# Optimization experiments

Measured on AMD Instinct MI355X. Metric: run time of the kernel, lower is better.

Reference implementation:

```python
import jax, jax.numpy as jnp
import numpy as np

B, S, D, OUT = 16, 2048, 64, 128

def setup_inputs() -> dict:
    key = jax.random.key(0)
    k1, k2, k3 = jax.random.split(key, 3)
    input_ = jax.random.normal(k1, (B, S, D), dtype=jnp.float32)
    # Linear(sequence_length -> output_features): W [out, S], b [out]
    W = jax.random.normal(k2, (OUT, S), dtype=jnp.float32) * (1.0 / np.sqrt(S))
    b = jax.random.normal(k3, (OUT,), dtype=jnp.float32) * 0.01
    return {"input_": input_, "W": W, "b": b}

def reference(input_, W, b):
    # Per-batch Gram matrix X @ X^T: [B, S, S]
    x_squared = jnp.einsum('bsd,btd->bst', input_, input_)
    # Linear over the last (sequence) dim: [B, S, out]
    out = jnp.einsum('bst,ot->bso', x_squared, W) + b
    return out
```

## Files before the change

### kernel.cpp

```cpp
#include <hip/hip_runtime.h>

#define BB 16
#define SS 2048
#define DD 64
#define OO 128
#define SPL 16
#define YN (BB * OO * DD)

typedef __attribute__((ext_vector_type(8))) short short8;
typedef __attribute__((ext_vector_type(4))) float f32x4;

__device__ __forceinline__ unsigned short f2bf(float f) {
    unsigned int u = __float_as_uint(f);
    return (unsigned short)((u + 0x7FFF + ((u >> 16) & 1)) >> 16);
}
__device__ __forceinline__ unsigned int pk2(float x, float y) {
    return (unsigned int)f2bf(x) | ((unsigned int)f2bf(y) << 16);
}
__device__ __forceinline__ short8 cvt8(float4 a, float4 b) {
    uint4 u = make_uint4(pk2(a.x, a.y), pk2(a.z, a.w), pk2(b.x, b.y), pk2(b.z, b.w));
    return *(short8*)&u;
}

__global__ __launch_bounds__(512) void k_yf(const float* __restrict__ X,
                                            const float* __restrict__ W,
                                            float* __restrict__ Yp) {
    __shared__ unsigned short XT[64 * 132];

    const int bx  = blockIdx.x;
    const int b   = bx & 15;
    const int p   = bx >> 4;
    const int t0  = p * (SS / SPL);
    const int tid = threadIdx.x;
    const int w   = tid >> 6;
    const int l   = tid & 63;

    const float* Xb = X + ((size_t)b * SS + t0) * DD;
#pragma unroll
    for (int i = 0; i < 4; ++i) {
        const int tl = w * 4 + i * 32;
        float x0 = Xb[(size_t)(tl + 0) * DD + l];
        float x1 = Xb[(size_t)(tl + 1) * DD + l];
        float x2 = Xb[(size_t)(tl + 2) * DD + l];
        float x3 = Xb[(size_t)(tl + 3) * DD + l];
        uint2 h  = make_uint2(pk2(x0, x1), pk2(x2, x3));
        *(uint2*)&XT[l * 132 + tl] = h;
    }
    __syncthreads();

    const int n = l & 15;
    const int q = l >> 4;

    f32x4 acc[4];
#pragma unroll
    for (int j = 0; j < 4; ++j) acc[j] = {0.f, 0.f, 0.f, 0.f};

    const int orow = w * 16 + n;
    const float* Wr = W + (size_t)orow * SS + t0;

#pragma unroll
    for (int kk = 0; kk < SS / SPL; kk += 32) {
        const float4 wa = *(const float4*)(Wr + kk + q * 8);
        const float4 wb = *(const float4*)(Wr + kk + q * 8 + 4);
        const short8 a  = cvt8(wa, wb);
#pragma unroll
        for (int j = 0; j < 4; ++j) {
            const unsigned short* r = &XT[(j * 16 + n) * 132 + kk + q * 8];
            uint2 lo = *(const uint2*)(r);
            uint2 hi = *(const uint2*)(r + 4);
            uint4 u  = make_uint4(lo.x, lo.y, hi.x, hi.y);
            acc[j] = __builtin_amdgcn_mfma_f32_16x16x32_bf16(a, *(short8*)&u, acc[j], 0, 0, 0);
        }
    }

    float* Yb = Yp + ((size_t)(p * BB + b) * OO + w * 16 + q * 4) * DD;
#pragma unroll
    for (int j = 0; j < 4; ++j)
#pragma unroll
        for (int r = 0; r < 4; ++r)
            Yb[(size_t)r * DD + j * 16 + n] = acc[j][r];
}

__global__ __launch_bounds__(512) void k_red(const float* __restrict__ Yp,
                                             float* __restrict__ Y) {
    const size_t i4 = ((size_t)blockIdx.x * 512 + threadIdx.x) * 4;
    float4 a = *(const float4*)(Yp + i4);
#pragma unroll
    for (int p = 1; p < SPL; ++p) {
        const float4 v = *(const float4*)(Yp + (size_t)p * YN + i4);
        a.x += v.x; a.y += v.y; a.z += v.z; a.w += v.w;
    }
    *(float4*)(Y + i4) = a;
}

__global__ __launch_bounds__(256, 2) void k_outf(const float* __restrict__ X,
                                                 const float* __restrict__ Y,
                                                 const float* __restrict__ bias,
                                                 float* __restrict__ out) {
    __shared__ unsigned short YL[OO * DD];

    const int bx  = blockIdx.x;
    const int b   = bx >> 5;
    const int s0  = (bx & 31) * 64;
    const int tid = threadIdx.x;
    const int w   = tid >> 6;
    const int l   = tid & 63;
    const int n   = l & 15;
    const int q   = l >> 4;

    const float* Yb = Y + (size_t)b * OO * DD;
#pragma unroll
    for (int i = 0; i < 8; ++i) {
        const int f = (tid + 256 * i) * 4;
        const float4 v = *(const float4*)(Yb + f);
        const int o = f >> 6, c = f & 63;
        const int e = o * 64 + ((((c >> 3) ^ (o & 7)) << 3) | (c & 7));
        *(uint2*)&YL[e] = make_uint2(pk2(v.x, v.y), pk2(v.z, v.w));
    }

    float bv[8];
#pragma unroll
    for (int j = 0; j < 8; ++j) bv[j] = bias[j * 16 + n];

    f32x4 acc[8];
#pragma unroll
    for (int j = 0; j < 8; ++j) acc[j] = {0.f, 0.f, 0.f, 0.f};

    __syncthreads();

    const int srow = s0 + w * 16 + n;
    const float* Xr = X + ((size_t)b * SS + srow) * DD;

#pragma unroll
    for (int kk = 0; kk < DD; kk += 32) {
        const float4 xa = *(const float4*)(Xr + kk + q * 8);
        const float4 xb = *(const float4*)(Xr + kk + q * 8 + 4);
        const short8 a  = cvt8(xa, xb);
        const int c8    = (kk >> 3) + q;
#pragma unroll
        for (int j = 0; j < 8; ++j) {
            const int o = j * 16 + n;
            const uint4 u = *(const uint4*)&YL[o * 64 + ((c8 ^ (o & 7)) << 3)];
            acc[j] = __builtin_amdgcn_mfma_f32_16x16x32_bf16(a, *(short8*)&u, acc[j], 0, 0, 0);
        }
    }

    float* op = out + ((size_t)b * SS + s0 + w * 16 + q * 4) * OO;
#pragma unroll
    for (int j = 0; j < 8; ++j)
#pragma unroll
        for (int r = 0; r < 4; ++r)
            op[(size_t)r * OO + j * 16 + n] = acc[j][r] + bv[j];
}

extern "C" void kernel_launch(void* const* d_in, const int* in_sizes, int n_in,
                              void* d_out, int out_size, void* d_ws, size_t ws_size,
                              hipStream_t stream) {
    const float* X    = (const float*)d_in[0];
    const float* W    = (const float*)d_in[1];
    const float* bias = (const float*)d_in[2];
    float* out = (float*)d_out;

    float* Yp = (float*)d_ws;
    float* Y  = Yp + (size_t)SPL * YN;

    k_yf <<<dim3(BB * SPL), dim3(512), 0, stream>>>(X, W, Yp);
    k_red<<<dim3(YN / 4 / 512), dim3(512), 0, stream>>>(Yp, Y);
    k_outf<<<dim3(512), dim3(256), 0, stream>>>(X, Y, bias, out);
}
```

Measured before the change: 80.18 us.

## Fuse three kernels into one cooperative kernel with grid syncs

Replaces the three launches (partial Y products, split reduction, output GEMM) with a single cooperative kernel of 256 blocks that separates the phases with grid.sync(). The reduction now writes Y directly as swizzled bf16 to global memory, and the output phase reads B operands from global instead of staging them in LDS, with each block handling 128 rows instead of 64. This removes launch gaps between kernels, but adds grid-barrier cost and leaves only 256 blocks for the output phase.

```diff
diff --git a/kernel.cpp b/kernel.cpp
--- a/kernel.cpp
+++ b/kernel.cpp
@@ -1,4 +1,5 @@
 #include <hip/hip_runtime.h>
+#include <hip/hip_cooperative_groups.h>
 
 #define BB 16
 #define SS 2048
@@ -22,135 +23,117 @@
     return *(short8*)&u;
 }
 
-__global__ __launch_bounds__(512) void k_yf(const float* __restrict__ X,
-                                            const float* __restrict__ W,
-                                            float* __restrict__ Yp) {
+__global__ __launch_bounds__(512) void k_all(const float* __restrict__ X,
+                                             const float* __restrict__ W,
+                                             const float* __restrict__ bias,
+                                             float* __restrict__ out,
+                                             float* __restrict__ Yp,
+                                             unsigned short* __restrict__ YB) {
+    cooperative_groups::grid_group grid = cooperative_groups::this_grid();
     __shared__ unsigned short XT[64 * 132];
 
     const int bx  = blockIdx.x;
-    const int b   = bx & 15;
-    const int p   = bx >> 4;
-    const int t0  = p * (SS / SPL);
-    const int tid = threadIdx.x;
-    const int w   = tid >> 6;
-    const int l   = tid & 63;
-
-    const float* Xb = X + ((size_t)b * SS + t0) * DD;
-#pragma unroll
-    for (int i = 0; i < 4; ++i) {
-        const int tl = w * 4 + i * 32;
-        float x0 = Xb[(size_t)(tl + 0) * DD + l];
-        float x1 = Xb[(size_t)(tl + 1) * DD + l];
-        float x2 = Xb[(size_t)(tl + 2) * DD + l];
-        float x3 = Xb[(size_t)(tl + 3) * DD + l];
-        uint2 h  = make_uint2(pk2(x0, x1), pk2(x2, x3));
-        *(uint2*)&XT[l * 132 + tl] = h;
-    }
-    __syncthreads();
-
-    const int n = l & 15;
-    const int q = l >> 4;
-
-    f32x4 acc[4];
-#pragma unroll
-    for (int j = 0; j < 4; ++j) acc[j] = {0.f, 0.f, 0.f, 0.f};
-
-    const int orow = w * 16 + n;
-    const float* Wr = W + (size_t)orow * SS + t0;
-
-#pragma unroll
-    for (int kk = 0; kk < SS / SPL; kk += 32) {
-        const float4 wa = *(const float4*)(Wr + kk + q * 8);
-        const float4 wb = *(const float4*)(Wr + kk + q * 8 + 4);
-        const short8 a  = cvt8(wa, wb);
-#pragma unroll
-        for (int j = 0; j < 4; ++j) {
-            const unsigned short* r = &XT[(j * 16 + n) * 132 + kk + q * 8];
-            uint2 lo = *(const uint2*)(r);
-            uint2 hi = *(const uint2*)(r + 4);
-            uint4 u  = make_uint4(lo.x, lo.y, hi.x, hi.y);
-            acc[j] = __builtin_amdgcn_mfma_f32_16x16x32_bf16(a, *(short8*)&u, acc[j], 0, 0, 0);
-        }
-    }
-
-    float* Yb = Yp + ((size_t)(p * BB + b) * OO + w * 16 + q * 4) * DD;
-#pragma unroll
-    for (int j = 0; j < 4; ++j)
-#pragma unroll
-        for (int r = 0; r < 4; ++r)
-            Yb[(size_t)r * DD + j * 16 + n] = acc[j][r];
-}
-
-__global__ __launch_bounds__(512) void k_red(const float* __restrict__ Yp,
-                                             float* __restrict__ Y) {
-    const size_t i4 = ((size_t)blockIdx.x * 512 + threadIdx.x) * 4;
-    float4 a = *(const float4*)(Yp + i4);
-#pragma unroll
-    for (int p = 1; p < SPL; ++p) {
-        const float4 v = *(const float4*)(Yp + (size_t)p * YN + i4);
-        a.x += v.x; a.y += v.y; a.z += v.z; a.w += v.w;
-    }
-    *(float4*)(Y + i4) = a;
-}
-
-__global__ __launch_bounds__(256, 2) void k_outf(const float* __restrict__ X,
-                                                 const float* __restrict__ Y,
-                                                 const float* __restrict__ bias,
-                                                 float* __restrict__ out) {
-    __shared__ unsigned short YL[OO * DD];
-
-    const int bx  = blockIdx.x;
-    const int b   = bx >> 5;
-    const int s0  = (bx & 31) * 64;
     const int tid = threadIdx.x;
     const int w   = tid >> 6;
     const int l   = tid & 63;
     const int n   = l & 15;
     const int q   = l >> 4;
 
-    const float* Yb = Y + (size_t)b * OO * DD;
+    {
+        const int b  = bx & 15;
+        const int p  = bx >> 4;
+        const int t0 = p * (SS / SPL);
+
+        const float* Xb = X + ((size_t)b * SS + t0) * DD;
 #pragma unroll
-    for (int i = 0; i < 8; ++i) {
-        const int f = (tid + 256 * i) * 4;
-        const float4 v = *(const float4*)(Yb + f);
-        const int o = f >> 6, c = f & 63;
-        const int e = o * 64 + ((((c >> 3) ^ (o & 7)) << 3) | (c & 7));
-        *(uint2*)&YL[e] = make_uint2(pk2(v.x, v.y), pk2(v.z, v.w));
+        for (int i = 0; i < 4; ++i) {
+            const int tl = w * 4 + i * 32;
+            float x0 = Xb[(size_t)(tl + 0) * DD + l];
+            float x1 = Xb[(size_t)(tl + 1) * DD + l];
+            float x2 = Xb[(size_t)(tl + 2) * DD + l];
+            float x3 = Xb[(size_t)(tl + 3) * DD + l];
+            *(uint2*)&XT[l * 132 + tl] = make_uint2(pk2(x0, x1), pk2(x2, x3));
+        }
+        __syncthreads();
+
+        f32x4 acc[4];
+#pragma unroll
+        for (int j = 0; j < 4; ++j) acc[j] = {0.f, 0.f, 0.f, 0.f};
+
+        const float* Wr = W + (size_t)(w * 16 + n) * SS + t0;
+#pragma unroll
+        for (int kk = 0; kk < SS / SPL; kk += 32) {
+            const float4 wa = *(const float4*)(Wr + kk + q * 8);
+            const float4 wb = *(const float4*)(Wr + kk + q * 8 + 4);
+            const short8 a  = cvt8(wa, wb);
+#pragma unroll
+            for (int j = 0; j < 4; ++j) {
+                const unsigned short* r = &XT[(j * 16 + n) * 132 + kk + q * 8];
+                uint2 lo = *(const uint2*)(r);
+                uint2 hi = *(const uint2*)(r + 4);
+                uint4 u  = make_uint4(lo.x, lo.y, hi.x, hi.y);
+                acc[j] = __builtin_amdgcn_mfma_f32_16x16x32_bf16(a, *(short8*)&u, acc[j], 0, 0, 0);
+            }
+        }
+
+        float* Yb = Yp + ((size_t)(p * BB + b) * OO + w * 16 + q * 4) * DD;
+#pragma unroll
+        for (int j = 0; j < 4; ++j)
+#pragma unroll
+            for (int r = 0; r < 4; ++r)
+                Yb[(size_t)r * DD + j * 16 + n] = acc[j][r];
     }
+    grid.sync();
 
-    float bv[8];
+    {
+        const int g = bx * 512 + tid;
+        float a = Yp[g];
 #pragma unroll
-    for (int j = 0; j < 8; ++j) bv[j] = bias[j * 16 + n];
+        for (int p = 1; p < SPL; ++p) a += Yp[(size_t)p * YN + g];
+        const int c = g & 63;
+        const int o = (g >> 6) & (OO - 1);
+        const int b = g >> 13;
+        const int e = ((b * OO + o) << 6) + ((((c >> 3) ^ (o & 7)) << 3) | (c & 7));
+        YB[e] = f2bf(a);
+    }
+    grid.sync();
 
-    f32x4 acc[8];
+    {
+        const int b  = bx >> 4;
+        const int s0 = (bx & 15) * 128;
+
+        float bv[8];
 #pragma unroll
-    for (int j = 0; j < 8; ++j) acc[j] = {0.f, 0.f, 0.f, 0.f};
+        for (int j = 0; j < 8; ++j) bv[j] = bias[j * 16 + n];
 
-    __syncthreads();
+        f32x4 acc[8];
+#pragma unroll
+        for (int j = 0; j < 8; ++j) acc[j] = {0.f, 0.f, 0.f, 0.f};
 
-    const int srow = s0 + w * 16 + n;
-    const float* Xr = X + ((size_t)b * SS + srow) * DD;
+        const float*          Xr  = X  + ((size_t)b * SS + s0 + w * 16 + n) * DD;
+        const unsigned short* Yb2 = YB + (size_t)b * OO * DD;
 
 #pragma unroll
-    for (int kk = 0; kk < DD; kk += 32) {
-        const float4 xa = *(const float4*)(Xr + kk + q * 8);
-        const float4 xb = *(const float4*)(Xr + kk + q * 8 + 4);
-        const short8 a  = cvt8(xa, xb);
-        const int c8    = (kk >> 3) + q;
+        for (int kk = 0; kk < DD; kk += 32) {
+            const float4 xa = *(const float4*)(Xr + kk + q * 8);
+            const float4 xb = *(const float4*)(Xr + kk + q * 8 + 4);
+            const short8 a  = cvt8(xa, xb);
+            const int c8    = (kk >> 3) + q;
 #pragma unroll
-        for (int j = 0; j < 8; ++j) {
-            const int o = j * 16 + n;
-            const uint4 u = *(const uint4*)&YL[o * 64 + ((c8 ^ (o & 7)) << 3)];
-            acc[j] = __builtin_amdgcn_mfma_f32_16x16x32_bf16(a, *(short8*)&u, acc[j], 0, 0, 0);
+            for (int j = 0; j < 8; ++j) {
+                const int o = j * 16 + n;
+                const uint4 u = *(const uint4*)(Yb2 + o * 64 + ((c8 ^ (o & 7)) << 3));
+                acc[j] = __builtin_amdgcn_mfma_f32_16x16x32_bf16(a, *(short8*)&u, acc[j], 0, 0, 0);
+            }
         }
+
+        float* op = out + ((size_t)b * SS + s0 + w * 16 + q * 4) * OO;
+#pragma unroll
+        for (int j = 0; j < 8; ++j)
+#pragma unroll
+            for (int r = 0; r < 4; ++r)
+                op[(size_t)r * OO + j * 16 + n] = acc[j][r] + bv[j];
     }
-
-    float* op = out + ((size_t)b * SS + s0 + w * 16 + q * 4) * OO;
-#pragma unroll
-    for (int j = 0; j < 8; ++j)
-#pragma unroll
-        for (int r = 0; r < 4; ++r)
-            op[(size_t)r * OO + j * 16 + n] = acc[j][r] + bv[j];
 }
 
 extern "C" void kernel_launch(void* const* d_in, const int* in_sizes, int n_in,
@@ -161,10 +144,11 @@
     const float* bias = (const float*)d_in[2];
     float* out = (float*)d_out;
 
-    float* Yp = (float*)d_ws;
-    float* Y  = Yp + (size_t)SPL * YN;
+    float*          Yp = (float*)d_ws;
+    unsigned short* YB = (unsigned short*)(Yp + (size_t)SPL * YN);
 
-    k_yf <<<dim3(BB * SPL), dim3(512), 0, stream>>>(X, W, Yp);
-    k_red<<<dim3(YN / 4 / 512), dim3(512), 0, stream>>>(Yp, Y);
-    k_outf<<<dim3(512), dim3(256), 0, stream>>>(X, Y, bias, out);
+    void* args[] = {(void*)&X, (void*)&W, (void*)&bias, (void*)&out,
+                    (void*)&Yp, (void*)&YB};
+    hipLaunchCooperativeKernel((const void*)k_all, dim3(256), dim3(512),
+                               args, 0, stream);
 }
```

After: 146.7 us. 1.83x slower.

## Fuse split-K reduction into output kernel with bf16 swizzled partials

Applied to the files above, without the earlier changes.

The first kernel now writes its split-K partial Y slabs as bf16, already in the XOR-swizzled layout the output GEMM uses. The separate reduction kernel is removed. Each output block sums the 16 partial slabs for its batch directly into shared memory before its MFMA loop. Output blocks now cover 128 rows with 512 threads. This removes a launch and halves partial traffic, at the cost of each of the 16 blocks per batch redundantly reducing the same partials, and extra rounding because partials are stored in bf16.

```diff
diff --git a/kernel.cpp b/kernel.cpp
--- a/kernel.cpp
+++ b/kernel.cpp
@@ -5,7 +5,7 @@
 #define DD 64
 #define OO 128
 #define SPL 16
-#define YN (BB * OO * DD)
+#define YEL (OO * DD)
 
 typedef __attribute__((ext_vector_type(8))) short short8;
 typedef __attribute__((ext_vector_type(4))) float f32x4;
@@ -21,10 +21,16 @@
     uint4 u = make_uint4(pk2(a.x, a.y), pk2(a.z, a.w), pk2(b.x, b.y), pk2(b.z, b.w));
     return *(short8*)&u;
 }
+__device__ __forceinline__ float bflo(unsigned int u) { return __uint_as_float(u << 16); }
+__device__ __forceinline__ float bfhi(unsigned int u) { return __uint_as_float(u & 0xffff0000u); }
+
+__device__ __forceinline__ int yswz(int o, int d) {
+    return (o << 6) + ((((d >> 3) ^ (o & 7)) << 3) | (d & 7));
+}
 
 __global__ __launch_bounds__(512) void k_yf(const float* __restrict__ X,
                                             const float* __restrict__ W,
-                                            float* __restrict__ Yp) {
+                                            unsigned short* __restrict__ YpB) {
     __shared__ unsigned short XT[64 * 132];
 
     const int bx  = blockIdx.x;
@@ -39,12 +45,11 @@
 #pragma unroll
     for (int i = 0; i < 4; ++i) {
         const int tl = w * 4 + i * 32;
-        float x0 = Xb[(size_t)(tl + 0) * DD + l];
-        float x1 = Xb[(size_t)(tl + 1) * DD + l];
-        float x2 = Xb[(size_t)(tl + 2) * DD + l];
-        float x3 = Xb[(size_t)(tl + 3) * DD + l];
-        uint2 h  = make_uint2(pk2(x0, x1), pk2(x2, x3));
-        *(uint2*)&XT[l * 132 + tl] = h;
+        const float x0 = Xb[(size_t)(tl + 0) * DD + l];
+        const float x1 = Xb[(size_t)(tl + 1) * DD + l];
+        const float x2 = Xb[(size_t)(tl + 2) * DD + l];
+        const float x3 = Xb[(size_t)(tl + 3) * DD + l];
+        *(uint2*)&XT[l * 132 + tl] = make_uint2(pk2(x0, x1), pk2(x2, x3));
     }
     __syncthreads();
 
@@ -55,9 +60,7 @@
 #pragma unroll
     for (int j = 0; j < 4; ++j) acc[j] = {0.f, 0.f, 0.f, 0.f};
 
-    const int orow = w * 16 + n;
-    const float* Wr = W + (size_t)orow * SS + t0;
-
+    const float* Wr = W + (size_t)(w * 16 + n) * SS + t0;
 #pragma unroll
     for (int kk = 0; kk < SS / SPL; kk += 32) {
         const float4 wa = *(const float4*)(Wr + kk + q * 8);
@@ -66,58 +69,55 @@
 #pragma unroll
         for (int j = 0; j < 4; ++j) {
             const unsigned short* r = &XT[(j * 16 + n) * 132 + kk + q * 8];
-            uint2 lo = *(const uint2*)(r);
-            uint2 hi = *(const uint2*)(r + 4);
-            uint4 u  = make_uint4(lo.x, lo.y, hi.x, hi.y);
+            const uint2 lo = *(const uint2*)(r);
+            const uint2 hi = *(const uint2*)(r + 4);
+            uint4 u = make_uint4(lo.x, lo.y, hi.x, hi.y);
             acc[j] = __builtin_amdgcn_mfma_f32_16x16x32_bf16(a, *(short8*)&u, acc[j], 0, 0, 0);
         }
     }
 
-    float* Yb = Yp + ((size_t)(p * BB + b) * OO + w * 16 + q * 4) * DD;
+    unsigned short* slab = YpB + (size_t)(b * SPL + p) * YEL;
 #pragma unroll
     for (int j = 0; j < 4; ++j)
 #pragma unroll
         for (int r = 0; r < 4; ++r)
-            Yb[(size_t)r * DD + j * 16 + n] = acc[j][r];
+            slab[yswz(w * 16 + q * 4 + r, j * 16 + n)] = f2bf(acc[j][r]);
 }
 
-__global__ __launch_bounds__(512) void k_red(const float* __restrict__ Yp,
-                                             float* __restrict__ Y) {
-    const size_t i4 = ((size_t)blockIdx.x * 512 + threadIdx.x) * 4;
-    float4 a = *(const float4*)(Yp + i4);
-#pragma unroll
-    for (int p = 1; p < SPL; ++p) {
-        const float4 v = *(const float4*)(Yp + (size_t)p * YN + i4);
-        a.x += v.x; a.y += v.y; a.z += v.z; a.w += v.w;
-    }
-    *(float4*)(Y + i4) = a;
-}
-
-__global__ __launch_bounds__(256, 2) void k_outf(const float* __restrict__ X,
-                                                 const float* __restrict__ Y,
-                                                 const float* __restrict__ bias,
-                                                 float* __restrict__ out) {
-    __shared__ unsigned short YL[OO * DD];
+__global__ __launch_bounds__(512) void k_out2(const float* __restrict__ X,
+                                              const unsigned short* __restrict__ YpB,
+                                              const float* __restrict__ bias,
+                                              float* __restrict__ out) {
+    __shared__ unsigned short YL[YEL];
 
     const int bx  = blockIdx.x;
-    const int b   = bx >> 5;
-    const int s0  = (bx & 31) * 64;
+    const int b   = bx & 15;
+    const int st  = bx >> 4;
     const int tid = threadIdx.x;
     const int w   = tid >> 6;
     const int l   = tid & 63;
     const int n   = l & 15;
     const int q   = l >> 4;
 
-    const float* Yb = Y + (size_t)b * OO * DD;
+    const uint4* Yb4 = (const uint4*)(YpB + (size_t)b * SPL * YEL);
 #pragma unroll
-    for (int i = 0; i < 8; ++i) {
-        const int f = (tid + 256 * i) * 4;
-        const float4 v = *(const float4*)(Yb + f);
-        const int o = f >> 6, c = f & 63;
-        const int e = o * 64 + ((((c >> 3) ^ (o & 7)) << 3) | (c & 7));
-        *(uint2*)&YL[e] = make_uint2(pk2(v.x, v.y), pk2(v.z, v.w));
+    for (int c = tid; c < YEL / 8; c += 512) {
+        float s[8];
+#pragma unroll
+        for (int e = 0; e < 8; ++e) s[e] = 0.f;
+#pragma unroll
+        for (int pp = 0; pp < SPL; ++pp) {
+            const uint4 v = Yb4[(size_t)pp * (YEL / 8) + c];
+            s[0] += bflo(v.x); s[1] += bfhi(v.x);
+            s[2] += bflo(v.y); s[3] += bfhi(v.y);
+            s[4] += bflo(v.z); s[5] += bfhi(v.z);
+            s[6] += bflo(v.w); s[7] += bfhi(v.w);
+        }
+        ((uint4*)YL)[c] = make_uint4(pk2(s[0], s[1]), pk2(s[2], s[3]),
+                                     pk2(s[4], s[5]), pk2(s[6], s[7]));
     }
 
+    const int s0 = st * 128;
     float bv[8];
 #pragma unroll
     for (int j = 0; j < 8; ++j) bv[j] = bias[j * 16 + n];
@@ -128,9 +128,7 @@
 
     __syncthreads();
 
-    const int srow = s0 + w * 16 + n;
-    const float* Xr = X + ((size_t)b * SS + srow) * DD;
-
+    const float* Xr = X + ((size_t)b * SS + s0 + w * 16 + n) * DD;
 #pragma unroll
     for (int kk = 0; kk < DD; kk += 32) {
         const float4 xa = *(const float4*)(Xr + kk + q * 8);
@@ -140,7 +138,7 @@
 #pragma unroll
         for (int j = 0; j < 8; ++j) {
             const int o = j * 16 + n;
-            const uint4 u = *(const uint4*)&YL[o * 64 + ((c8 ^ (o & 7)) << 3)];
+            const uint4 u = *(const uint4*)&YL[(o << 6) + (((c8 ^ (o & 7)) << 3))];
             acc[j] = __builtin_amdgcn_mfma_f32_16x16x32_bf16(a, *(short8*)&u, acc[j], 0, 0, 0);
         }
     }
@@ -161,10 +159,8 @@
     const float* bias = (const float*)d_in[2];
     float* out = (float*)d_out;
 
-    float* Yp = (float*)d_ws;
-    float* Y  = Yp + (size_t)SPL * YN;
+    unsigned short* YpB = (unsigned short*)d_ws;
 
-    k_yf <<<dim3(BB * SPL), dim3(512), 0, stream>>>(X, W, Yp);
-    k_red<<<dim3(YN / 4 / 512), dim3(512), 0, stream>>>(Yp, Y);
-    k_outf<<<dim3(512), dim3(256), 0, stream>>>(X, Y, bias, out);
+    k_yf <<<dim3(256), dim3(512), 0, stream>>>(X, W, YpB);
+    k_out2<<<dim3(256), dim3(512), 0, stream>>>(X, YpB, bias, out);
 }
```

New measurement: 76.93 us. -4.0%, faster.
